# Performance work log

Measured on AMD Instinct MI355X. Metric: run time of the kernel, lower is better.

The kernel has to match this reference:

```python
import jax, jax.numpy as jnp
import numpy as np

NUM_HEADS = 8
HEAD_DIM = 64
EPEG_K = 5
SCALE = HEAD_DIM ** -0.5


def setup_inputs() -> dict:
    key = jax.random.key(0)
    ks = jax.random.split(key, 7)
    B, N, C = 2, 2048, 512
    H, D = NUM_HEADS, HEAD_DIM
    x = jax.random.normal(ks[0], (B, N, C), dtype=jnp.float32)
    w_qkv = jax.random.normal(ks[1], (3 * H * D, C), dtype=jnp.float32) * 0.02
    b_qkv = jax.random.normal(ks[2], (3 * H * D,), dtype=jnp.float32) * 0.02
    w_proj = jax.random.normal(ks[3], (C, H * D), dtype=jnp.float32) * 0.02
    b_proj = jax.random.normal(ks[4], (C,), dtype=jnp.float32) * 0.02
    conv_w = jax.random.normal(ks[5], (H, 1, EPEG_K, 1), dtype=jnp.float32) * 0.1
    conv_b = jax.random.normal(ks[6], (H,), dtype=jnp.float32) * 0.1
    return {"x": x, "w_qkv": w_qkv, "b_qkv": b_qkv, "w_proj": w_proj,
            "b_proj": b_proj, "conv_w": conv_w, "conv_b": conv_b}


def reference(x, w_qkv, b_qkv, w_proj, b_proj, conv_w, conv_b):
    B, N, C = x.shape
    H, D = NUM_HEADS, HEAD_DIM
    pad = EPEG_K // 2
    # fused QKV projection: [B,N,3*H*D] -> [3,B,H,N,D]
    qkv = (jnp.einsum('bnc,fc->bnf', x, w_qkv) + b_qkv)
    qkv = qkv.reshape(B, N, 3, H, D).transpose(2, 0, 3, 1, 4)
    q, k, v = qkv[0], qkv[1], qkv[2]
    # attention scores [B,H,N,N]
    attn = jnp.einsum('bhqd,bhkd->bhqk', q * SCALE, k)
    # EPEG: depthwise conv over heads with kernel (k,1) along the query axis
    conv = jax.lax.conv_general_dilated(
        attn, conv_w, window_strides=(1, 1), padding=((pad, pad), (0, 0)),
        dimension_numbers=('NCHW', 'OIHW', 'NCHW'), feature_group_count=H)
    attn = attn + conv + conv_b[None, :, None, None]
    attn = jax.nn.softmax(attn, axis=-1)
    out = jnp.einsum('bhqk,bhkd->bhqd', attn, v)
    out = out.transpose(0, 2, 1, 3).reshape(B, N, H * D)
    return jnp.einsum('bnf,cf->bnc', out, w_proj) + b_proj
```

## Files before the change

kernel.cpp:

```cpp
#include <hip/hip_runtime.h>
#include <hip/hip_bf16.h>
#include <cstdint>
#include <cstddef>

#define NB 2
#define NN 2048
#define NC 512
#define NH 8
#define ND 64
#define NF3 1536
#define ATT_SCALE 0.125f
#define LOG2E 1.44269504088896340736f

typedef __bf16 bf16x8 __attribute__((ext_vector_type(8)));
typedef unsigned short u16x8 __attribute__((ext_vector_type(8)));
typedef float f32x4 __attribute__((ext_vector_type(4)));

__device__ __forceinline__ unsigned short f2bf(float f){
  unsigned int u = __builtin_bit_cast(unsigned int, f);
  u += 0x7fffu + ((u >> 16) & 1u);
  return (unsigned short)(u >> 16);
}
__device__ __forceinline__ float bf2f(unsigned short s){
  unsigned int u = ((unsigned int)s) << 16;
  return __builtin_bit_cast(float, u);
}
__device__ __forceinline__ unsigned int pkbf2(float lo, float hi){
  return (unsigned int)f2bf(lo) | ((unsigned int)f2bf(hi) << 16);
}
__device__ __forceinline__ unsigned int cvtpk_bf2(float lo, float hi){
  unsigned int r;
  asm("v_cvt_pk_bf16_f32 %0, %1, %2" : "=v"(r) : "v"(lo), "v"(hi));
  return r;
}
__device__ __forceinline__ float exp2_hw(float x){
  float r;
  asm("v_exp_f32 %0, %1" : "=v"(r) : "v"(x));
  return r;
}

__device__ __forceinline__ bf16x8 ldfrag(const void* p){
  return __builtin_bit_cast(bf16x8, *(const u16x8*)p);
}

__device__ __forceinline__ void gload16(const void* g, void* l){
  __builtin_amdgcn_global_load_lds((const __attribute__((address_space(1))) unsigned int*)g,
                                   (__attribute__((address_space(3))) unsigned int*)l, 16, 0, 0);
}

__global__ void f2bf3_kernel(const float* __restrict__ a, unsigned short* __restrict__ oa, int na,
                             const float* __restrict__ b, unsigned short* __restrict__ ob, int nb,
                             const float* __restrict__ c, unsigned short* __restrict__ oc, int nc){
  int i = (blockIdx.x * 256 + threadIdx.x) * 4;
  const float* src; unsigned short* dst; int off;
  if (i < na)            { src = a; dst = oa; off = i; }
  else if (i < na + nb)  { src = b; dst = ob; off = i - na; }
  else if (i < na+nb+nc) { src = c; dst = oc; off = i - na - nb; }
  else return;
  float4 v = *(const float4*)(src + off);
  *(uint2*)(dst + off) = make_uint2(pkbf2(v.x, v.y), pkbf2(v.z, v.w));
}

template<int EPI>
__global__ __launch_bounds__(256, 2) void gemm_bt(
    const unsigned short* __restrict__ A, const unsigned short* __restrict__ Bm,
    const float* __restrict__ bias, float* __restrict__ outF,
    unsigned short* __restrict__ Qb, unsigned short* __restrict__ Kb,
    unsigned short* __restrict__ Vb, int M, int Nn, int K)
{
  __shared__ unsigned short As[128*32];
  __shared__ unsigned short Bs[128*32];
  const int tid = threadIdx.x;
  const int w = tid >> 6, l = tid & 63;
  const int bm = blockIdx.x, bn = blockIdx.y;
  const int wr = (w >> 1) * 64, wc = (w & 1) * 64;
  const int l4 = l >> 4, l15 = l & 15;

  f32x4 acc[4][4];
  #pragma unroll
  for (int i=0;i<4;i++)
    #pragma unroll
    for (int j=0;j<4;j++)
      #pragma unroll
      for (int r=0;r<4;r++) acc[i][j][r] = 0.f;

  const int KT = K >> 5;
  for (int kt = 0; kt < KT; ++kt){
    const int kc = kt << 5;
    #pragma unroll
    for (int c = 0; c < 2; ++c){
      const int rbase = w*32 + c*16;
      gload16(A  + (size_t)(bm*128 + rbase + (l>>2))*K + kc + (l&3)*8, &As[rbase*32]);
      gload16(Bm + (size_t)(bn*128 + rbase + (l>>2))*K + kc + (l&3)*8, &Bs[rbase*32]);
    }
    __syncthreads();
    bf16x8 af[4], bfr[4];
    #pragma unroll
    for (int mf=0;mf<4;mf++) af[mf]  = ldfrag(&As[(wr + mf*16 + l15)*32 + l4*8]);
    #pragma unroll
    for (int nf=0;nf<4;nf++) bfr[nf] = ldfrag(&Bs[(wc + nf*16 + l15)*32 + l4*8]);
    #pragma unroll
    for (int mf=0;mf<4;mf++)
      #pragma unroll
      for (int nf=0;nf<4;nf++)
        acc[mf][nf] = __builtin_amdgcn_mfma_f32_16x16x32_bf16(af[mf], bfr[nf], acc[mf][nf], 0, 0, 0);
    __syncthreads();
  }

  #pragma unroll
  for (int mf=0;mf<4;mf++){
    #pragma unroll
    for (int nf=0;nf<4;nf++){
      const int col = bn*128 + wc + nf*16 + l15;
      const float bv = bias[col];
      const int rowb = bm*128 + wr + mf*16 + l4*4;
      if (EPI == 0){
        #pragma unroll
        for (int r=0;r<4;r++)
          outF[(size_t)(rowb + r) * Nn + col] = acc[mf][nf][r] + bv;
      } else {
        const int s = col >> 9, hh = (col >> 6) & 7, d = col & 63;
        const int b = rowb >> 11, n = rowb & 2047;
        if (s == 2){
          *(uint2*)&Vb[(((size_t)b*NH + hh)*ND + d)*NN + n] =
            make_uint2(pkbf2(acc[mf][nf][0]+bv, acc[mf][nf][1]+bv),
                       pkbf2(acc[mf][nf][2]+bv, acc[mf][nf][3]+bv));
        } else {
          unsigned short* dst = (s == 0) ? Qb : Kb;
          const float sc = (s == 0) ? ATT_SCALE : 1.f;
          #pragma unroll
          for (int r=0;r<4;r++)
            dst[(((size_t)b*NH + hh)*NN + (n + r))*ND + d] = f2bf((acc[mf][nf][r]+bv)*sc);
        }
      }
    }
  }
}

__global__ __launch_bounds__(512, 4) void attn_kernel(
    const unsigned short* __restrict__ Qb, const unsigned short* __restrict__ Kb,
    const unsigned short* __restrict__ Vb, const float* __restrict__ conv_w,
    const float* __restrict__ conv_b, unsigned short* __restrict__ AO)
{
  __shared__ __align__(16) char smem[65536];
  unsigned short* Klds = (unsigned short*)smem;
  unsigned short* Vlds = (unsigned short*)(smem + 32768);
  float* comb = (float*)smem;

  const int tid = threadIdx.x;
  const int w = tid >> 6, l = tid & 63;
  const int g = w >> 2, wq = w & 3;
  const int l4 = l >> 4, l15 = l & 15;
  const int qt = blockIdx.x, bh = blockIdx.y;
  const int h = bh & 7;
  const int q0 = qt * 64;
  const unsigned short* Qg = Qb + (size_t)bh * NN * ND;
  const unsigned short* Kg = Kb + (size_t)bh * NN * ND;
  const unsigned short* Vg = Vb + (size_t)bh * ND * NN;
  float cw[5];
  #pragma unroll
  for (int o=0;o<5;o++) cw[o] = conv_w[h*5+o] * LOG2E;
  cw[2] += LOG2E;

  bf16x8 qf[2];
  {
    const int q = q0 + wq*16 + l15;
    #pragma unroll
    for (int kc2=0;kc2<2;kc2++){
      float a8[8];
      #pragma unroll
      for (int j=0;j<8;j++) a8[j] = 0.f;
      #pragma unroll
      for (int o=0;o<5;o++){
        const int qg = q - 2 + o;
        if (qg >= 0 && qg < NN){
          u16x8 v = *(const u16x8*)(Qg + (size_t)qg*ND + kc2*32 + l4*8);
          #pragma unroll
          for (int j=0;j<8;j++) a8[j] = fmaf(cw[o], bf2f(v[j]), a8[j]);
        }
      }
      u16x8 pk;
      #pragma unroll
      for (int j=0;j<8;j++) pk[j] = f2bf(a8[j]);
      qf[kc2] = __builtin_bit_cast(bf16x8, pk);
    }
  }

  const int srow0 = wq*16 + (l>>3);
  const int scg   = (l&7) ^ (l>>3);
  const int soffK = scg * 8;
  const int soffV = ((scg & 4) | ((scg & 1) << 1) | ((scg >> 1) & 1)) * 8;
  #define STAGE_KV(bufi, k0s)                                                                     \
    gload16(Kg + (size_t)((k0s) + srow0    )*ND + soffK, &Klds[((g*2+(bufi))*64 + wq*16    )*64]); \
    gload16(Kg + (size_t)((k0s) + srow0 + 8)*ND + soffK, &Klds[((g*2+(bufi))*64 + wq*16 + 8)*64]); \
    gload16(Vg + (size_t)(srow0    )*NN + (k0s) + soffV, &Vlds[((g*2+(bufi))*64 + wq*16    )*64]); \
    gload16(Vg + (size_t)(srow0 + 8)*NN + (k0s) + soffV, &Vlds[((g*2+(bufi))*64 + wq*16 + 8)*64]);

  STAGE_KV(0, g*64)

  f32x4 oacc[4];
  #pragma unroll
  for (int i=0;i<4;i++)
    #pragma unroll
    for (int r=0;r<4;r++) oacc[i][r] = 0.f;
  float l_st = 0.f;

  const int sz = (l15 & 7) << 4;
  const bool ue = (l4 & 1);

  __syncthreads();

  for (int it = 0; it < 16; ++it){
    const int buf = it & 1;
    const int kbase = (g*2+buf)*64*64;
    if (it + 1 < 16){ STAGE_KV(buf^1, (2*(it+1)+g)*64) }

    f32x4 sacc[4];
    __builtin_amdgcn_s_setprio(1);
    #pragma unroll
    for (int kf=0;kf<4;kf++){
      const char* kb = (const char*)&Klds[kbase] + (kf*16 + l15)*128;
      bf16x8 k0f = ldfrag(kb + ((l4*16)      ^ sz));
      bf16x8 k1f = ldfrag(kb + ((64 + l4*16) ^ sz));
      f32x4 s;
      #pragma unroll
      for (int r=0;r<4;r++) s[r] = 0.f;
      s = __builtin_amdgcn_mfma_f32_16x16x32_bf16(k0f, qf[0], s, 0,0,0);
      sacc[kf] = __builtin_amdgcn_mfma_f32_16x16x32_bf16(k1f, qf[1], s, 0,0,0);
    }
    __builtin_amdgcn_s_setprio(0);

    bf16x8 vf[4][2];
    #pragma unroll
    for (int df=0;df<4;df++){
      const char* vb = (const char*)&Vlds[kbase] + (df*16 + l15)*128;
      vf[df][0] = ldfrag(vb + ((l4*16)      ^ sz));
      vf[df][1] = ldfrag(vb + ((64 + l4*16) ^ sz));
    }

    float p16[16];
    #pragma unroll
    for (int kf=0;kf<4;kf++)
      #pragma unroll
      for (int r=0;r<4;r++) p16[kf*4+r] = exp2_hw(sacc[kf][r]);
    {
      float ps = 0.f;
      #pragma unroll
      for (int i=0;i<16;i++) ps += p16[i];
      l_st += ps;
    }

    unsigned int pk8[8];
    #pragma unroll
    for (int kf=0;kf<4;kf++)
      #pragma unroll
      for (int j=0;j<2;j++)
        pk8[2*kf+j] = cvtpk_bf2(p16[kf*4+2*j], p16[kf*4+2*j+1]);

    const unsigned int r1 = (unsigned int)__shfl_xor((int)(ue ? pk8[0] : pk8[2]), 16);
    const unsigned int r2 = (unsigned int)__shfl_xor((int)(ue ? pk8[1] : pk8[3]), 16);
    const unsigned int r3 = (unsigned int)__shfl_xor((int)(ue ? pk8[4] : pk8[6]), 16);
    const unsigned int r4 = (unsigned int)__shfl_xor((int)(ue ? pk8[5] : pk8[7]), 16);
    const uint4 b0u = ue ? make_uint4(r1, r2, pk8[2], pk8[3])
                         : make_uint4(pk8[0], pk8[1], r1, r2);
    const uint4 b1u = ue ? make_uint4(r3, r4, pk8[6], pk8[7])
                         : make_uint4(pk8[4], pk8[5], r3, r4);
    const bf16x8 pb0 = __builtin_bit_cast(bf16x8, b0u);
    const bf16x8 pb1 = __builtin_bit_cast(bf16x8, b1u);

    __builtin_amdgcn_s_setprio(1);
    #pragma unroll
    for (int df=0;df<4;df++){
      oacc[df] = __builtin_amdgcn_mfma_f32_16x16x32_bf16(vf[df][0], pb0, oacc[df], 0,0,0);
      oacc[df] = __builtin_amdgcn_mfma_f32_16x16x32_bf16(vf[df][1], pb1, oacc[df], 0,0,0);
    }
    __builtin_amdgcn_s_setprio(0);
    __syncthreads();
  }

  l_st += __shfl_xor(l_st, 16);
  l_st += __shfl_xor(l_st, 32);

  if (g == 1){
    float* pb = comb + ((size_t)(wq*64 + l))*17;
    #pragma unroll
    for (int df=0;df<4;df++)
      #pragma unroll
      for (int r=0;r<4;r++) pb[df*4+r] = oacc[df][r];
    pb[16] = l_st;
  }
  __syncthreads();
  if (g == 0){
    const float* pb = comb + ((size_t)(wq*64 + l))*17;
    #pragma unroll
    for (int df=0;df<4;df++)
      #pragma unroll
      for (int r=0;r<4;r++) oacc[df][r] += pb[df*4+r];
    l_st += pb[16];

    const float inv = 1.f / l_st;
    const int b = bh >> 3;
    const int q = q0 + wq*16 + l15;
    unsigned short* aoq = AO + ((size_t)(b*NN + q))*NC + h*64;
    #pragma unroll
    for (int df=0;df<4;df++)
      *(uint2*)(aoq + df*16 + l4*4) =
        make_uint2(pkbf2(oacc[df][0]*inv, oacc[df][1]*inv),
                   pkbf2(oacc[df][2]*inv, oacc[df][3]*inv));
  }
}

extern "C" void kernel_launch(void* const* d_in, const int* in_sizes, int n_in,
                              void* d_out, int out_size, void* d_ws, size_t ws_size,
                              hipStream_t stream)
{
  const float* x      = (const float*)d_in[0];
  const float* w_qkv  = (const float*)d_in[1];
  const float* b_qkv  = (const float*)d_in[2];
  const float* w_proj = (const float*)d_in[3];
  const float* b_proj = (const float*)d_in[4];
  const float* conv_w = (const float*)d_in[5];
  const float* conv_b = (const float*)d_in[6];
  float* out = (float*)d_out;

  char* ws = (char*)d_ws;
  unsigned short* xb     = (unsigned short*)(ws);
  unsigned short* wqkvb  = (unsigned short*)(ws + 4194304);
  unsigned short* wprojb = (unsigned short*)(ws + 5767168);
  unsigned short* Qb     = (unsigned short*)(ws + 6291456);
  unsigned short* Kb     = (unsigned short*)(ws + 10485760);
  unsigned short* Vb     = (unsigned short*)(ws + 14680064);
  unsigned short* AO     = (unsigned short*)(ws + 18874368);

  f2bf3_kernel<<<3072, 256, 0, stream>>>(x, xb, NB*NN*NC,
                                         w_qkv, wqkvb, NF3*NC,
                                         w_proj, wprojb, NC*NC);

  gemm_bt<1><<<dim3(32,12), 256, 0, stream>>>(xb, wqkvb, b_qkv, nullptr,
                                              Qb, Kb, Vb, NB*NN, NF3, NC);

  attn_kernel<<<dim3(32,16), 512, 0, stream>>>(Qb, Kb, Vb, conv_w, conv_b, AO);

  gemm_bt<0><<<dim3(32,4), 256, 0, stream>>>(AO, wprojb, b_proj, out,
                                             nullptr, nullptr, nullptr, NB*NN, NC, NC);
}
```

Before: 69.78 us.

## Halve attention block to 4 waves, each computing two 16-row query subtiles

```diff
diff --git a/kernel.cpp b/kernel.cpp
--- a/kernel.cpp
+++ b/kernel.cpp
@@ -137,7 +137,7 @@
   }
 }
 
-__global__ __launch_bounds__(512, 4) void attn_kernel(
+__global__ __launch_bounds__(256, 2) void attn_kernel(
     const unsigned short* __restrict__ Qb, const unsigned short* __restrict__ Kb,
     const unsigned short* __restrict__ Vb, const float* __restrict__ conv_w,
     const float* __restrict__ conv_b, unsigned short* __restrict__ AO)
@@ -149,7 +149,7 @@
 
   const int tid = threadIdx.x;
   const int w = tid >> 6, l = tid & 63;
-  const int g = w >> 2, wq = w & 3;
+  const int g = w >> 1, wq = w & 1;
   const int l4 = l >> 4, l15 = l & 15;
   const int qt = blockIdx.x, bh = blockIdx.y;
   const int h = bh & 7;
@@ -162,9 +162,10 @@
   for (int o=0;o<5;o++) cw[o] = conv_w[h*5+o] * LOG2E;
   cw[2] += LOG2E;
 
-  bf16x8 qf[2];
-  {
-    const int q = q0 + wq*16 + l15;
+  bf16x8 qf[2][2];
+  #pragma unroll
+  for (int sub=0;sub<2;sub++){
+    const int q = q0 + wq*32 + sub*16 + l15;
     #pragma unroll
     for (int kc2=0;kc2<2;kc2++){
       float a8[8];
@@ -182,28 +183,31 @@
       u16x8 pk;
       #pragma unroll
       for (int j=0;j<8;j++) pk[j] = f2bf(a8[j]);
-      qf[kc2] = __builtin_bit_cast(bf16x8, pk);
-    }
-  }
-
-  const int srow0 = wq*16 + (l>>3);
+      qf[sub][kc2] = __builtin_bit_cast(bf16x8, pk);
+    }
+  }
+
+  const int srow0 = wq*32 + (l>>3);
   const int scg   = (l&7) ^ (l>>3);
   const int soffK = scg * 8;
   const int soffV = ((scg & 4) | ((scg & 1) << 1) | ((scg >> 1) & 1)) * 8;
-  #define STAGE_KV(bufi, k0s)                                                                     \
-    gload16(Kg + (size_t)((k0s) + srow0    )*ND + soffK, &Klds[((g*2+(bufi))*64 + wq*16    )*64]); \
-    gload16(Kg + (size_t)((k0s) + srow0 + 8)*ND + soffK, &Klds[((g*2+(bufi))*64 + wq*16 + 8)*64]); \
-    gload16(Vg + (size_t)(srow0    )*NN + (k0s) + soffV, &Vlds[((g*2+(bufi))*64 + wq*16    )*64]); \
-    gload16(Vg + (size_t)(srow0 + 8)*NN + (k0s) + soffV, &Vlds[((g*2+(bufi))*64 + wq*16 + 8)*64]);
+  #define STAGE_KV(bufi, k0s)                                                                          \
+    _Pragma("unroll")                                                                                  \
+    for (int c = 0; c < 4; ++c){                                                                       \
+      gload16(Kg + (size_t)((k0s) + srow0 + c*8)*ND + soffK, &Klds[((g*2+(bufi))*64 + wq*32 + c*8)*64]); \
+      gload16(Vg + (size_t)(srow0 + c*8)*NN + (k0s) + soffV, &Vlds[((g*2+(bufi))*64 + wq*32 + c*8)*64]); \
+    }
 
   STAGE_KV(0, g*64)
 
-  f32x4 oacc[4];
-  #pragma unroll
-  for (int i=0;i<4;i++)
-    #pragma unroll
-    for (int r=0;r<4;r++) oacc[i][r] = 0.f;
-  float l_st = 0.f;
+  f32x4 oacc[2][4];
+  #pragma unroll
+  for (int s2=0;s2<2;s2++)
+    #pragma unroll
+    for (int i=0;i<4;i++)
+      #pragma unroll
+      for (int r=0;r<4;r++) oacc[s2][i][r] = 0.f;
+  float l_st0 = 0.f, l_st1 = 0.f;
 
   const int sz = (l15 & 7) << 4;
   const bool ue = (l4 & 1);
@@ -215,18 +219,21 @@
     const int kbase = (g*2+buf)*64*64;
     if (it + 1 < 16){ STAGE_KV(buf^1, (2*(it+1)+g)*64) }
 
-    f32x4 sacc[4];
+    f32x4 sacc[2][4];
     __builtin_amdgcn_s_setprio(1);
     #pragma unroll
     for (int kf=0;kf<4;kf++){
       const char* kb = (const char*)&Klds[kbase] + (kf*16 + l15)*128;
       bf16x8 k0f = ldfrag(kb + ((l4*16)      ^ sz));
       bf16x8 k1f = ldfrag(kb + ((64 + l4*16) ^ sz));
-      f32x4 s;
-      #pragma unroll
-      for (int r=0;r<4;r++) s[r] = 0.f;
-      s = __builtin_amdgcn_mfma_f32_16x16x32_bf16(k0f, qf[0], s, 0,0,0);
-      sacc[kf] = __builtin_amdgcn_mfma_f32_16x16x32_bf16(k1f, qf[1], s, 0,0,0);
+      #pragma unroll
+      for (int sub=0;sub<2;sub++){
+        f32x4 s;
+        #pragma unroll
+        for (int r=0;r<4;r++) s[r] = 0.f;
+        s = __builtin_amdgcn_mfma_f32_16x16x32_bf16(k0f, qf[sub][0], s, 0,0,0);
+        sacc[sub][kf] = __builtin_amdgcn_mfma_f32_16x16x32_bf16(k1f, qf[sub][1], s, 0,0,0);
+      }
     }
     __builtin_amdgcn_s_setprio(0);
 
@@ -238,75 +245,91 @@
       vf[df][1] = ldfrag(vb + ((64 + l4*16) ^ sz));
     }
 
-    float p16[16];
-    #pragma unroll
-    for (int kf=0;kf<4;kf++)
-      #pragma unroll
-      for (int r=0;r<4;r++) p16[kf*4+r] = exp2_hw(sacc[kf][r]);
-    {
+    bf16x8 pb0[2], pb1[2];
+    #pragma unroll
+    for (int sub=0;sub<2;sub++){
+      float p16[16];
+      #pragma unroll
+      for (int kf=0;kf<4;kf++)
+        #pragma unroll
+        for (int r=0;r<4;r++) p16[kf*4+r] = exp2_hw(sacc[sub][kf][r]);
       float ps = 0.f;
       #pragma unroll
       for (int i=0;i<16;i++) ps += p16[i];
-      l_st += ps;
-    }
-
-    unsigned int pk8[8];
-    #pragma unroll
-    for (int kf=0;kf<4;kf++)
-      #pragma unroll
-      for (int j=0;j<2;j++)
-        pk8[2*kf+j] = cvtpk_bf2(p16[kf*4+2*j], p16[kf*4+2*j+1]);
-
-    const unsigned int r1 = (unsigned int)__shfl_xor((int)(ue ? pk8[0] : pk8[2]), 16);
-    const unsigned int r2 = (unsigned int)__shfl_xor((int)(ue ? pk8[1] : pk8[3]), 16);
-    const unsigned int r3 = (unsigned int)__shfl_xor((int)(ue ? pk8[4] : pk8[6]), 16);
-    const unsigned int r4 = (unsigned int)__shfl_xor((int)(ue ? pk8[5] : pk8[7]), 16);
-    const uint4 b0u = ue ? make_uint4(r1, r2, pk8[2], pk8[3])
-                         : make_uint4(pk8[0], pk8[1], r1, r2);
-    const uint4 b1u = ue ? make_uint4(r3, r4, pk8[6], pk8[7])
-                         : make_uint4(pk8[4], pk8[5], r3, r4);
-    const bf16x8 pb0 = __builtin_bit_cast(bf16x8, b0u);
-    const bf16x8 pb1 = __builtin_bit_cast(bf16x8, b1u);
+      if (sub == 0) l_st0 += ps; else l_st1 += ps;
+
+      unsigned int pk8[8];
+      #pragma unroll
+      for (int kf=0;kf<4;kf++)
+        #pragma unroll
+        for (int j=0;j<2;j++)
+          pk8[2*kf+j] = cvtpk_bf2(p16[kf*4+2*j], p16[kf*4+2*j+1]);
+
+      const unsigned int r1 = (unsigned int)__shfl_xor((int)(ue ? pk8[0] : pk8[2]), 16);
+      const unsigned int r2 = (unsigned int)__shfl_xor((int)(ue ? pk8[1] : pk8[3]), 16);
+      const unsigned int r3 = (unsigned int)__shfl_xor((int)(ue ? pk8[4] : pk8[6]), 16);
+      const unsigned int r4 = (unsigned int)__shfl_xor((int)(ue ? pk8[5] : pk8[7]), 16);
+      const uint4 b0u = ue ? make_uint4(r1, r2, pk8[2], pk8[3])
+                           : make_uint4(pk8[0], pk8[1], r1, r2);
+      const uint4 b1u = ue ? make_uint4(r3, r4, pk8[6], pk8[7])
+                           : make_uint4(pk8[4], pk8[5], r3, r4);
+      pb0[sub] = __builtin_bit_cast(bf16x8, b0u);
+      pb1[sub] = __builtin_bit_cast(bf16x8, b1u);
+    }
 
     __builtin_amdgcn_s_setprio(1);
     #pragma unroll
     for (int df=0;df<4;df++){
-      oacc[df] = __builtin_amdgcn_mfma_f32_16x16x32_bf16(vf[df][0], pb0, oacc[df], 0,0,0);
-      oacc[df] = __builtin_amdgcn_mfma_f32_16x16x32_bf16(vf[df][1], pb1, oacc[df], 0,0,0);
+      #pragma unroll
+      for (int sub=0;sub<2;sub++){
+        oacc[sub][df] = __builtin_amdgcn_mfma_f32_16x16x32_bf16(vf[df][0], pb0[sub], oacc[sub][df], 0,0,0);
+        oacc[sub][df] = __builtin_amdgcn_mfma_f32_16x16x32_bf16(vf[df][1], pb1[sub], oacc[sub][df], 0,0,0);
+      }
     }
     __builtin_amdgcn_s_setprio(0);
     __syncthreads();
   }
 
-  l_st += __shfl_xor(l_st, 16);
-  l_st += __shfl_xor(l_st, 32);
+  l_st0 += __shfl_xor(l_st0, 16);
+  l_st0 += __shfl_xor(l_st0, 32);
+  l_st1 += __shfl_xor(l_st1, 16);
+  l_st1 += __shfl_xor(l_st1, 32);
 
   if (g == 1){
-    float* pb = comb + ((size_t)(wq*64 + l))*17;
-    #pragma unroll
-    for (int df=0;df<4;df++)
-      #pragma unroll
-      for (int r=0;r<4;r++) pb[df*4+r] = oacc[df][r];
-    pb[16] = l_st;
+    float* pb = comb + ((size_t)(wq*64 + l))*34;
+    #pragma unroll
+    for (int s2=0;s2<2;s2++)
+      #pragma unroll
+      for (int df=0;df<4;df++)
+        #pragma unroll
+        for (int r=0;r<4;r++) pb[s2*16 + df*4+r] = oacc[s2][df][r];
+    pb[32] = l_st0;
+    pb[33] = l_st1;
   }
   __syncthreads();
   if (g == 0){
-    const float* pb = comb + ((size_t)(wq*64 + l))*17;
-    #pragma unroll
-    for (int df=0;df<4;df++)
-      #pragma unroll
-      for (int r=0;r<4;r++) oacc[df][r] += pb[df*4+r];
-    l_st += pb[16];
-
-    const float inv = 1.f / l_st;
+    const float* pb = comb + ((size_t)(wq*64 + l))*34;
+    #pragma unroll
+    for (int s2=0;s2<2;s2++)
+      #pragma unroll
+      for (int df=0;df<4;df++)
+        #pragma unroll
+        for (int r=0;r<4;r++) oacc[s2][df][r] += pb[s2*16 + df*4+r];
+    l_st0 += pb[32];
+    l_st1 += pb[33];
+
     const int b = bh >> 3;
-    const int q = q0 + wq*16 + l15;
-    unsigned short* aoq = AO + ((size_t)(b*NN + q))*NC + h*64;
-    #pragma unroll
-    for (int df=0;df<4;df++)
-      *(uint2*)(aoq + df*16 + l4*4) =
-        make_uint2(pkbf2(oacc[df][0]*inv, oacc[df][1]*inv),
-                   pkbf2(oacc[df][2]*inv, oacc[df][3]*inv));
+    #pragma unroll
+    for (int sub=0;sub<2;sub++){
+      const float inv = 1.f / (sub == 0 ? l_st0 : l_st1);
+      const int q = q0 + wq*32 + sub*16 + l15;
+      unsigned short* aoq = AO + ((size_t)(b*NN + q))*NC + h*64;
+      #pragma unroll
+      for (int df=0;df<4;df++)
+        *(uint2*)(aoq + df*16 + l4*4) =
+          make_uint2(pkbf2(oacc[sub][df][0]*inv, oacc[sub][df][1]*inv),
+                     pkbf2(oacc[sub][df][2]*inv, oacc[sub][df][3]*inv));
+    }
   }
 }
 
@@ -339,7 +362,7 @@
   gemm_bt<1><<<dim3(32,12), 256, 0, stream>>>(xb, wqkvb, b_qkv, nullptr,
                                               Qb, Kb, Vb, NB*NN, NF3, NC);
 
-  attn_kernel<<<dim3(32,16), 512, 0, stream>>>(Qb, Kb, Vb, conv_w, conv_b, AO);
+  attn_kernel<<<dim3(32,16), 256, 0, stream>>>(Qb, Kb, Vb, conv_w, conv_b, AO);
 
   gemm_bt<0><<<dim3(32,4), 256, 0, stream>>>(AO, wprojb, b_proj, out,
                                              nullptr, nullptr, nullptr, NB*NN, NC, NC);
```

New measurement: 72.84 us. +4.4%, slower.

## Halve attention key tile to 32 to cut LDS and raise occupancy

Applied to the files above, without the earlier changes.

```diff
diff --git a/kernel.cpp b/kernel.cpp
--- a/kernel.cpp
+++ b/kernel.cpp
@@ -137,14 +137,14 @@
   }
 }
 
-__global__ __launch_bounds__(512, 4) void attn_kernel(
+__global__ __launch_bounds__(512, 8) void attn_kernel(
     const unsigned short* __restrict__ Qb, const unsigned short* __restrict__ Kb,
     const unsigned short* __restrict__ Vb, const float* __restrict__ conv_w,
     const float* __restrict__ conv_b, unsigned short* __restrict__ AO)
 {
-  __shared__ __align__(16) char smem[65536];
+  __shared__ __align__(16) char smem[32768];
   unsigned short* Klds = (unsigned short*)smem;
-  unsigned short* Vlds = (unsigned short*)(smem + 32768);
+  unsigned short* Vlds = (unsigned short*)(smem + 16384);
   float* comb = (float*)smem;
 
   const int tid = threadIdx.x;
@@ -186,17 +186,16 @@
     }
   }
 
-  const int srow0 = wq*16 + (l>>3);
-  const int scg   = (l&7) ^ (l>>3);
-  const int soffK = scg * 8;
-  const int soffV = ((scg & 4) | ((scg & 1) << 1) | ((scg >> 1) & 1)) * 8;
-  #define STAGE_KV(bufi, k0s)                                                                     \
-    gload16(Kg + (size_t)((k0s) + srow0    )*ND + soffK, &Klds[((g*2+(bufi))*64 + wq*16    )*64]); \
-    gload16(Kg + (size_t)((k0s) + srow0 + 8)*ND + soffK, &Klds[((g*2+(bufi))*64 + wq*16 + 8)*64]); \
-    gload16(Vg + (size_t)(srow0    )*NN + (k0s) + soffV, &Vlds[((g*2+(bufi))*64 + wq*16    )*64]); \
-    gload16(Vg + (size_t)(srow0 + 8)*NN + (k0s) + soffV, &Vlds[((g*2+(bufi))*64 + wq*16 + 8)*64]);
-
-  STAGE_KV(0, g*64)
+  const int krow = wq*8 + (l>>3);
+  const int ksrc = ((l&7) ^ (l>>3)) * 8;
+  const int vrow = wq*16 + (l>>2);
+  const int vsg  = (l&3) ^ ((l>>2)&3);
+  const int vsrc = (((vsg&1)<<1) | (vsg>>1)) * 8;
+  #define STAGE_KV(bufi, k0s)                                                        \
+    gload16(Kg + (size_t)((k0s) + krow)*ND + ksrc, &Klds[((g*2+(bufi))*32 + wq*8)*64]); \
+    gload16(Vg + (size_t)vrow*NN + (k0s) + vsrc,   &Vlds[((g*2+(bufi))*64 + wq*16)*32]);
+
+  STAGE_KV(0, g*32)
 
   f32x4 oacc[4];
   #pragma unroll
@@ -205,23 +204,25 @@
     for (int r=0;r<4;r++) oacc[i][r] = 0.f;
   float l_st = 0.f;
 
-  const int sz = (l15 & 7) << 4;
+  const int szk = (l15 & 7) << 4;
+  const int szv = (l15 & 3) << 4;
   const bool ue = (l4 & 1);
 
   __syncthreads();
 
-  for (int it = 0; it < 16; ++it){
+  for (int it = 0; it < 32; ++it){
     const int buf = it & 1;
-    const int kbase = (g*2+buf)*64*64;
-    if (it + 1 < 16){ STAGE_KV(buf^1, (2*(it+1)+g)*64) }
-
-    f32x4 sacc[4];
+    const int kb0 = (g*2+buf)*32*64;
+    const int vb0 = (g*2+buf)*64*32;
+    if (it + 1 < 32){ STAGE_KV(buf^1, (2*(it+1)+g)*32) }
+
+    f32x4 sacc[2];
     __builtin_amdgcn_s_setprio(1);
     #pragma unroll
-    for (int kf=0;kf<4;kf++){
-      const char* kb = (const char*)&Klds[kbase] + (kf*16 + l15)*128;
-      bf16x8 k0f = ldfrag(kb + ((l4*16)      ^ sz));
-      bf16x8 k1f = ldfrag(kb + ((64 + l4*16) ^ sz));
+    for (int kf=0;kf<2;kf++){
+      const char* kb = (const char*)&Klds[kb0] + (kf*16 + l15)*128;
+      bf16x8 k0f = ldfrag(kb + ((l4*16)      ^ szk));
+      bf16x8 k1f = ldfrag(kb + ((64 + l4*16) ^ szk));
       f32x4 s;
       #pragma unroll
       for (int r=0;r<4;r++) s[r] = 0.f;
@@ -230,50 +231,39 @@
     }
     __builtin_amdgcn_s_setprio(0);
 
-    bf16x8 vf[4][2];
+    bf16x8 vf[4];
     #pragma unroll
     for (int df=0;df<4;df++){
-      const char* vb = (const char*)&Vlds[kbase] + (df*16 + l15)*128;
-      vf[df][0] = ldfrag(vb + ((l4*16)      ^ sz));
-      vf[df][1] = ldfrag(vb + ((64 + l4*16) ^ sz));
-    }
-
-    float p16[16];
-    #pragma unroll
-    for (int kf=0;kf<4;kf++)
-      #pragma unroll
-      for (int r=0;r<4;r++) p16[kf*4+r] = exp2_hw(sacc[kf][r]);
+      const char* vb = (const char*)&Vlds[vb0] + (df*16 + l15)*64;
+      vf[df] = ldfrag(vb + ((l4*16) ^ szv));
+    }
+
+    float p8[8];
+    #pragma unroll
+    for (int kf=0;kf<2;kf++)
+      #pragma unroll
+      for (int r=0;r<4;r++) p8[kf*4+r] = exp2_hw(sacc[kf][r]);
     {
       float ps = 0.f;
       #pragma unroll
-      for (int i=0;i<16;i++) ps += p16[i];
+      for (int i=0;i<8;i++) ps += p8[i];
       l_st += ps;
     }
-
-    unsigned int pk8[8];
-    #pragma unroll
-    for (int kf=0;kf<4;kf++)
-      #pragma unroll
-      for (int j=0;j<2;j++)
-        pk8[2*kf+j] = cvtpk_bf2(p16[kf*4+2*j], p16[kf*4+2*j+1]);
-
-    const unsigned int r1 = (unsigned int)__shfl_xor((int)(ue ? pk8[0] : pk8[2]), 16);
-    const unsigned int r2 = (unsigned int)__shfl_xor((int)(ue ? pk8[1] : pk8[3]), 16);
-    const unsigned int r3 = (unsigned int)__shfl_xor((int)(ue ? pk8[4] : pk8[6]), 16);
-    const unsigned int r4 = (unsigned int)__shfl_xor((int)(ue ? pk8[5] : pk8[7]), 16);
-    const uint4 b0u = ue ? make_uint4(r1, r2, pk8[2], pk8[3])
-                         : make_uint4(pk8[0], pk8[1], r1, r2);
-    const uint4 b1u = ue ? make_uint4(r3, r4, pk8[6], pk8[7])
-                         : make_uint4(pk8[4], pk8[5], r3, r4);
+    const unsigned int pkA = cvtpk_bf2(p8[0], p8[1]);
+    const unsigned int pkB = cvtpk_bf2(p8[2], p8[3]);
+    const unsigned int pkC = cvtpk_bf2(p8[4], p8[5]);
+    const unsigned int pkD = cvtpk_bf2(p8[6], p8[7]);
+
+    const unsigned int t1 = (unsigned int)__shfl_xor((int)(ue ? pkA : pkC), 16);
+    const unsigned int t2 = (unsigned int)__shfl_xor((int)(ue ? pkB : pkD), 16);
+    const uint4 b0u = ue ? make_uint4(t1, t2, pkC, pkD)
+                         : make_uint4(pkA, pkB, t1, t2);
     const bf16x8 pb0 = __builtin_bit_cast(bf16x8, b0u);
-    const bf16x8 pb1 = __builtin_bit_cast(bf16x8, b1u);
 
     __builtin_amdgcn_s_setprio(1);
     #pragma unroll
-    for (int df=0;df<4;df++){
-      oacc[df] = __builtin_amdgcn_mfma_f32_16x16x32_bf16(vf[df][0], pb0, oacc[df], 0,0,0);
-      oacc[df] = __builtin_amdgcn_mfma_f32_16x16x32_bf16(vf[df][1], pb1, oacc[df], 0,0,0);
-    }
+    for (int df=0;df<4;df++)
+      oacc[df] = __builtin_amdgcn_mfma_f32_16x16x32_bf16(vf[df], pb0, oacc[df], 0,0,0);
     __builtin_amdgcn_s_setprio(0);
     __syncthreads();
   }
```

After: 73.41 us. +5.2%, slower.
